# Optimization experiments

Hardware: AMD Instinct MI355X
Metric: run time of the kernel (lower is better)

Reference implementation:

```python
import jax, jax.numpy as jnp
import numpy as np

EPS = 1e-5
H = 8
N_BUCKETS = 32


def _instance_norm(x, gamma, beta):
    # x: [B, N, D]; torch InstanceNorm1d normalizes over the N (length) dim
    # per channel per batch element, using biased variance.
    m = jnp.mean(x, axis=1, keepdims=True)
    v = jnp.var(x, axis=1, keepdims=True)
    return (x - m) * jax.lax.rsqrt(v + EPS) * gamma + beta


def setup_inputs() -> dict:
    key = jax.random.key(0)
    ks = jax.random.split(key, 12)
    B, N, D, d_ff = 4, 512, 128, 512
    s = 1.0 / np.sqrt(D)
    sf = 1.0 / np.sqrt(d_ff)
    u = lambda k, shape, lim: jax.random.uniform(k, shape, jnp.float32, -lim, lim)
    return {
        "h": jax.random.normal(ks[0], (B, N, D), jnp.float32),
        "coords": jax.random.uniform(ks[1], (B, N, 2), jnp.float32),
        "W_Q": u(ks[2], (D, D), s),
        "W_K": u(ks[3], (D, D), s),
        "W_V": u(ks[4], (D, D), s),
        "W_O": u(ks[5], (D, D), s),
        "emb": jax.random.normal(ks[6], (N_BUCKETS, D), jnp.float32),  # n_heads*d_k == D
        "ffn_w1": u(ks[7], (D, d_ff), s),
        "ffn_b1": u(ks[8], (d_ff,), s),
        "ffn_w2": u(ks[9], (d_ff, D), sf),
        "ffn_b2": u(ks[10], (D,), sf),
        "gamma1": jnp.ones((D,), jnp.float32),
        "beta1": jnp.zeros((D,), jnp.float32),
        "gamma2": jnp.ones((D,), jnp.float32),
        "beta2": jnp.zeros((D,), jnp.float32),
    }


def reference(h, coords, W_Q, W_K, W_V, W_O, emb, ffn_w1, ffn_b1, ffn_w2,
              ffn_b2, gamma1, beta1, gamma2, beta2):
    B, N, D = h.shape
    Dk = D // H
    Q = (h @ W_Q).reshape(B, N, H, Dk)
    K = (h @ W_K).reshape(B, N, H, Dk)
    V = (h @ W_V).reshape(B, N, H, Dk)
    # content scores: [B, H, N, N]
    scores = jnp.einsum('bnhd,bmhd->bhnm', Q, K) / np.sqrt(Dk)
    # relative-distance bucket embeddings for all (i, j) pairs
    diff = coords[:, :, None, :] - coords[:, None, :, :]          # [B,N,N,2]
    dist = jax.lax.stop_gradient(jnp.sqrt(jnp.sum(diff * diff, -1)))
    buckets = jnp.clip((dist * N_BUCKETS).astype(jnp.int32), 0, N_BUCKETS - 1)
    r = emb[buckets].reshape(B, N, N, H, Dk)                      # [B,N,N,H,Dk]
    scores = scores + jnp.einsum('bnhd,bnmhd->bhnm', Q, r)
    attn = jax.nn.softmax(scores, axis=-1)
    h_attn = jnp.einsum('bhnm,bmhd->bnhd', attn, V).reshape(B, N, D) @ W_O
    h1 = _instance_norm(h + h_attn, gamma1, beta1)
    h_ffn = jax.nn.relu(h1 @ ffn_w1 + ffn_b1) @ ffn_w2 + ffn_b2
    return _instance_norm(h1 + h_ffn, gamma2, beta2)
```

## Files before the change

### kernel.cpp

```cpp
#include <hip/hip_runtime.h>
#include <hip/hip_bf16.h>

#define B_  4
#define N_  512
#define D_  128
#define H_  8
#define DK  16
#define DFF 512
#define NB  32
#define KS  8
#define FS  8

__global__ __launch_bounds__(256) void qkv_qe_kernel(
    const float* __restrict__ A,
    const float* __restrict__ WQ, const float* __restrict__ WK, const float* __restrict__ WV,
    const float* __restrict__ emb,
    float* __restrict__ Qo, float* __restrict__ Ko, float* __restrict__ Vo,
    float* __restrict__ QE)
{
    const float* Bw = blockIdx.z == 0 ? WQ : (blockIdx.z == 1 ? WK : WV);
    float*       C  = blockIdx.z == 0 ? Qo : (blockIdx.z == 1 ? Ko : Vo);
    const int wave = threadIdx.x >> 6;
    const int lane = threadIdx.x & 63;
    const int rbase = __builtin_amdgcn_readfirstlane((blockIdx.x * 4 + wave) * 4);
    const int col = lane * 2;

    float acc[4][2] = {};
#pragma unroll 2
    for (int k0 = 0; k0 < D_; k0 += 4) {
        float4 a4[4];
#pragma unroll
        for (int j = 0; j < 4; ++j)
            a4[j] = *(const float4*)&A[(size_t)(rbase + j) * D_ + k0];
#pragma unroll
        for (int kk = 0; kk < 4; ++kk) {
            float2 bv = *(const float2*)&Bw[(size_t)(k0 + kk) * D_ + col];
#pragma unroll
            for (int j = 0; j < 4; ++j) {
                float a = (&a4[j].x)[kk];
                acc[j][0] += a * bv.x;
                acc[j][1] += a * bv.y;
            }
        }
    }
#pragma unroll
    for (int j = 0; j < 4; ++j)
        *(float2*)&C[(size_t)(rbase + j) * D_ + col] = make_float2(acc[j][0], acc[j][1]);

    if (blockIdx.z == 0) {
        __shared__ float Qls[16][132];
#pragma unroll
        for (int j = 0; j < 4; ++j)
            *(float2*)&Qls[wave * 4 + j][col] = make_float2(acc[j][0], acc[j][1]);
        __syncthreads();
        const int r  = threadIdx.x >> 4;
        const int hh = (threadIdx.x & 15) >> 1;
        const int k0 = (threadIdx.x & 1) * 16;
        const int grow = blockIdx.x * 16 + r;
        const float4* qv = (const float4*)&Qls[r][hh * DK];
        const float4 qa = qv[0], qb = qv[1], qc = qv[2], qd = qv[3];
        float* qe_out = QE + ((size_t)grow * H_ + hh) * NB + k0;
#pragma unroll 4
        for (int k = 0; k < 16; ++k) {
            const float4* ep = (const float4*)(emb + (size_t)(k0 + k) * D_ + hh * DK);
            float4 e0 = ep[0], e1 = ep[1], e2 = ep[2], e3 = ep[3];
            float dot = qa.x*e0.x + qa.y*e0.y + qa.z*e0.z + qa.w*e0.w
                      + qb.x*e1.x + qb.y*e1.y + qb.z*e1.z + qb.w*e1.w
                      + qc.x*e2.x + qc.y*e2.y + qc.z*e2.z + qc.w*e2.w
                      + qd.x*e3.x + qd.y*e3.y + qd.z*e3.z + qd.w*e3.w;
            qe_out[k] = dot;
        }
    }
}

__global__ __launch_bounds__(256) void attn5_kernel(
    const float* __restrict__ Q, const float* __restrict__ K, const float* __restrict__ V,
    const float* __restrict__ QE, const float* __restrict__ coords,
    float* __restrict__ P)
{
    const int tid  = threadIdx.x;
    const int wave = tid >> 6;
    const int lane = tid & 63;
    const int bid  = blockIdx.x;
    const int ks    = bid & 7;
    const int chunk = (bid >> 3) & 7;
    const int h     = (bid >> 6) & (H_ - 1);
    const int b     = bid >> 9;

    const int n   = chunk * 64 + lane;
    const int row = b * N_ + n;

    __shared__ float qel[64][NB + 1];
    __shared__ float ckrd[64][2];
    __shared__ float accl[4][64][17];

    {
        int r = tid >> 2, part = tid & 3;
        const float* src = QE + ((size_t)(b * N_ + chunk * 64 + r) * H_ + h) * NB + part * 8;
#pragma unroll
        for (int j = 0; j < 8; ++j) qel[r][part * 8 + j] = src[j];
    }
    if (tid < 128)
        ((float*)ckrd)[tid] = coords[(size_t)(b * N_ + ks * 64) * 2 + tid];

    const float4* qp = (const float4*)(Q + (size_t)row * D_ + h * DK);
    const float4 q0 = qp[0], q1 = qp[1], q2 = qp[2], q3 = qp[3];
    const float cx = coords[(size_t)row * 2 + 0];
    const float cy = coords[(size_t)row * 2 + 1];

    __syncthreads();

    const size_t hdbase = (size_t)b * N_ * D_ + h * DK;

    float l = 0.f;
    float acc[16] = {};

    const int m0 = __builtin_amdgcn_readfirstlane(ks * 64 + wave * 16);
#pragma unroll 4
    for (int i = 0; i < 16; ++i) {
        const int m = m0 + i;
        const float4* kp = (const float4*)(K + hdbase + (size_t)m * D_);
        const float4 k0 = kp[0], k1 = kp[1], k2 = kp[2], k3 = kp[3];
        float dot = q0.x*k0.x + q0.y*k0.y + q0.z*k0.z + q0.w*k0.w
                  + q1.x*k1.x + q1.y*k1.y + q1.z*k1.z + q1.w*k1.w
                  + q2.x*k2.x + q2.y*k2.y + q2.z*k2.z + q2.w*k2.w
                  + q3.x*k3.x + q3.y*k3.y + q3.z*k3.z + q3.w*k3.w;
        const int mloc = m - ks * 64;
        float dx = cx - ckrd[mloc][0], dy = cy - ckrd[mloc][1];
        float dist = sqrtf(dx * dx + dy * dy);
        int bucket = (int)(dist * 32.0f);
        bucket = bucket > (NB - 1) ? (NB - 1) : bucket;
        float s = dot * 0.25f + qel[lane][bucket];
        float p = __expf(s);
        l += p;
        const float4* vp = (const float4*)(V + hdbase + (size_t)m * D_);
        const float4 v0 = vp[0], v1 = vp[1], v2 = vp[2], v3 = vp[3];
        acc[0]  += p * v0.x; acc[1]  += p * v0.y; acc[2]  += p * v0.z; acc[3]  += p * v0.w;
        acc[4]  += p * v1.x; acc[5]  += p * v1.y; acc[6]  += p * v1.z; acc[7]  += p * v1.w;
        acc[8]  += p * v2.x; acc[9]  += p * v2.y; acc[10] += p * v2.z; acc[11] += p * v2.w;
        acc[12] += p * v3.x; acc[13] += p * v3.y; acc[14] += p * v3.z; acc[15] += p * v3.w;
    }

    accl[wave][lane][16] = l;
#pragma unroll
    for (int j = 0; j < 16; ++j) accl[wave][lane][j] = acc[j];
    __syncthreads();

    float* pb = P + (size_t)bid * (64 * 17);
    for (int i = tid; i < 64 * 17; i += 256) {
        int r = i / 17, j = i - r * 17;
        pb[i] = accl[0][r][j] + accl[1][r][j] + accl[2][r][j] + accl[3][r][j];
    }
}

__global__ __launch_bounds__(256) void oproj_kernel(
    const float* __restrict__ P, const float* __restrict__ WO,
    const float* __restrict__ hres, float* __restrict__ X1)
{
    const int tid = threadIdx.x;
    const int gr0 = blockIdx.x * 16;
    __shared__ float AOls[16][128];
    __shared__ float lsl[16][8];

    if (tid < 128) {
        int r = tid >> 3, hh = tid & 7;
        int gr = gr0 + r;
        int b = gr >> 9, n = gr & (N_ - 1);
        int chunk = n >> 6, rl = n & 63;
        size_t base = ((size_t)(((b * H_ + hh) * 8 + chunk) * KS)) * (64 * 17) + (size_t)rl * 17;
        float l = 0.f;
#pragma unroll
        for (int s = 0; s < KS; ++s) l += P[base + (size_t)s * (64 * 17) + 16];
        lsl[r][hh] = l;
    }

    float asum[8];
#pragma unroll
    for (int j = 0; j < 8; ++j) {
        int i = tid + j * 256;
        int r = i >> 7, d = i & 127;
        int gr = gr0 + r;
        int b = gr >> 9, n = gr & (N_ - 1);
        int chunk = n >> 6, rl = n & 63;
        int hh = d >> 4, dk = d & 15;
        size_t base = ((size_t)(((b * H_ + hh) * 8 + chunk) * KS)) * (64 * 17) + (size_t)rl * 17 + dk;
        float a = 0.f;
#pragma unroll
        for (int s = 0; s < KS; ++s) a += P[base + (size_t)s * (64 * 17)];
        asum[j] = a;
    }
    __syncthreads();
#pragma unroll
    for (int j = 0; j < 8; ++j) {
        int i = tid + j * 256;
        int r = i >> 7, d = i & 127;
        AOls[r][d] = asum[j] / lsl[r][d >> 4];
    }
    __syncthreads();

    const int wave = tid >> 6;
    const int lane = tid & 63;
    const int rl = wave * 4;
    const int grb = __builtin_amdgcn_readfirstlane(gr0 + rl);
    const int col = lane * 2;

    float acc[4][2] = {};
#pragma unroll 2
    for (int k0 = 0; k0 < D_; k0 += 4) {
        float4 a4[4];
#pragma unroll
        for (int j = 0; j < 4; ++j) a4[j] = *(const float4*)&AOls[rl + j][k0];
#pragma unroll
        for (int kk = 0; kk < 4; ++kk) {
            float2 bv = *(const float2*)&WO[(size_t)(k0 + kk) * D_ + col];
#pragma unroll
            for (int j = 0; j < 4; ++j) {
                float a = (&a4[j].x)[kk];
                acc[j][0] += a * bv.x;
                acc[j][1] += a * bv.y;
            }
        }
    }
#pragma unroll
    for (int j = 0; j < 4; ++j) {
        float2 rv = *(const float2*)&hres[(size_t)(grb + j) * D_ + col];
        *(float2*)&X1[(size_t)(grb + j) * D_ + col] =
            make_float2(acc[j][0] + rv.x, acc[j][1] + rv.y);
    }
}

__global__ __launch_bounds__(256) void stats_kernel(const float* __restrict__ X,
    const float* __restrict__ gamma, const float* __restrict__ beta,
    float* __restrict__ T1, float* __restrict__ T2)
{
    const int b  = blockIdx.x >> 3;
    const int dg = blockIdx.x & 7;
    const int dl = threadIdx.x & 15;
    const int nc = threadIdx.x >> 4;
    const int d  = dg * 16 + dl;
    const float* xb = X + (size_t)b * N_ * D_ + d;
    float s = 0.f, q = 0.f;
    for (int i = 0; i < 32; ++i) {
        float x = xb[(size_t)(nc * 32 + i) * D_];
        s += x; q += x * x;
    }
    __shared__ float ls[16][17], lq[16][17];
    ls[nc][dl] = s; lq[nc][dl] = q;
    __syncthreads();
    if (threadIdx.x < 16) {
        float S = 0.f, Q2 = 0.f;
#pragma unroll
        for (int i = 0; i < 16; ++i) { S += ls[i][threadIdx.x]; Q2 += lq[i][threadIdx.x]; }
        int dd = dg * 16 + threadIdx.x;
        float mean = S * (1.0f / N_);
        float var  = Q2 * (1.0f / N_) - mean * mean;
        float r = 1.0f / sqrtf(var + 1e-5f);
        float t1 = r * gamma[dd];
        T1[b * D_ + dd] = t1;
        T2[b * D_ + dd] = beta[dd] - mean * t1;
    }
}

__global__ __launch_bounds__(256) void ffn1_kernel(
    const float* __restrict__ X1, const float* __restrict__ T1, const float* __restrict__ T2,
    const float* __restrict__ w1, const float* __restrict__ b1, float* __restrict__ F1)
{
    __shared__ float Als[32][128];
    const int gr0 = blockIdx.x * 32;
    const int b = gr0 >> 9;
    for (int i = threadIdx.x * 4; i < 32 * 128; i += 1024) {
        int r = i >> 7, c = i & 127;
        float4 x  = *(const float4*)&X1[(size_t)(gr0 + r) * D_ + c];
        float4 t1 = *(const float4*)&T1[b * D_ + c];
        float4 t2 = *(const float4*)&T2[b * D_ + c];
        float4 y;
        y.x = x.x * t1.x + t2.x; y.y = x.y * t1.y + t2.y;
        y.z = x.z * t1.z + t2.z; y.w = x.w * t1.w + t2.w;
        *(float4*)&Als[r][c] = y;
    }
    __syncthreads();

    const int wave = threadIdx.x >> 6;
    const int lane = threadIdx.x & 63;
    const int rl = wave * 8;
    const int grb = __builtin_amdgcn_readfirstlane(gr0 + rl);
    const int col = blockIdx.y * 128 + lane * 2;

    float acc[8][2] = {};
#pragma unroll 2
    for (int k0 = 0; k0 < D_; k0 += 4) {
        float4 a4[8];
#pragma unroll
        for (int j = 0; j < 8; ++j) a4[j] = *(const float4*)&Als[rl + j][k0];
#pragma unroll
        for (int kk = 0; kk < 4; ++kk) {
            float2 bv = *(const float2*)&w1[(size_t)(k0 + kk) * DFF + col];
#pragma unroll
            for (int j = 0; j < 8; ++j) {
                float a = (&a4[j].x)[kk];
                acc[j][0] += a * bv.x;
                acc[j][1] += a * bv.y;
            }
        }
    }
    float2 bb = *(const float2*)&b1[col];
#pragma unroll
    for (int j = 0; j < 8; ++j) {
        float o0 = fmaxf(acc[j][0] + bb.x, 0.f);
        float o1 = fmaxf(acc[j][1] + bb.y, 0.f);
        *(float2*)&F1[(size_t)(grb + j) * DFF + col] = make_float2(o0, o1);
    }
}

__global__ __launch_bounds__(256) void ffn2s_kernel(
    const float* __restrict__ F1, const float* __restrict__ w2, float* __restrict__ Pf)
{
    const int wave = threadIdx.x >> 6;
    const int lane = threadIdx.x & 63;
    const int rbase = __builtin_amdgcn_readfirstlane((blockIdx.x * 4 + wave) * 8);
    const int col = lane * 2;
    const int s = blockIdx.z;
    const int kbeg = s * (DFF / FS);

    float acc[8][2] = {};
#pragma unroll 2
    for (int k0 = kbeg; k0 < kbeg + DFF / FS; k0 += 4) {
        float4 a4[8];
#pragma unroll
        for (int j = 0; j < 8; ++j)
            a4[j] = *(const float4*)&F1[(size_t)(rbase + j) * DFF + k0];
#pragma unroll
        for (int kk = 0; kk < 4; ++kk) {
            float2 bv = *(const float2*)&w2[(size_t)(k0 + kk) * D_ + col];
#pragma unroll
            for (int j = 0; j < 8; ++j) {
                float a = (&a4[j].x)[kk];
                acc[j][0] += a * bv.x;
                acc[j][1] += a * bv.y;
            }
        }
    }
#pragma unroll
    for (int j = 0; j < 8; ++j)
        *(float2*)&Pf[((size_t)s * (B_ * N_) + rbase + j) * D_ + col] =
            make_float2(acc[j][0], acc[j][1]);
}

__global__ __launch_bounds__(256) void fcomb_kernel(
    const float* __restrict__ Pf, const float* __restrict__ b2,
    const float* __restrict__ X1, const float* __restrict__ T1, const float* __restrict__ T2,
    float* __restrict__ X2)
{
    int idx = (blockIdx.x * 256 + threadIdx.x) * 4;
    int d = idx & (D_ - 1);
    int b = idx >> 16;
    float4 o  = *(const float4*)&b2[d];
    float4 x1 = *(const float4*)&X1[idx];
    float4 t1 = *(const float4*)&T1[b * D_ + d];
    float4 t2 = *(const float4*)&T2[b * D_ + d];
    o.x += x1.x * t1.x + t2.x; o.y += x1.y * t1.y + t2.y;
    o.z += x1.z * t1.z + t2.z; o.w += x1.w * t1.w + t2.w;
#pragma unroll
    for (int s = 0; s < FS; ++s) {
        float4 p = *(const float4*)&Pf[(size_t)s * (B_ * N_ * D_) + idx];
        o.x += p.x; o.y += p.y; o.z += p.z; o.w += p.w;
    }
    *(float4*)&X2[idx] = o;
}

__global__ __launch_bounds__(256) void stats_apply_kernel(const float* __restrict__ X,
    const float* __restrict__ gamma, const float* __restrict__ beta,
    float* __restrict__ Y)
{
    const int b  = blockIdx.x >> 3;
    const int dg = blockIdx.x & 7;
    const int dl = threadIdx.x & 15;
    const int nc = threadIdx.x >> 4;
    const int d  = dg * 16 + dl;
    const float* xb = X + (size_t)b * N_ * D_ + d;
    float s = 0.f, q = 0.f;
#pragma unroll 4
    for (int i = 0; i < 32; ++i) {
        float x = xb[(size_t)(nc * 32 + i) * D_];
        s += x; q += x * x;
    }
    __shared__ float ls[16][17], lq[16][17];
    __shared__ float t1l[16], t2l[16];
    ls[nc][dl] = s; lq[nc][dl] = q;
    __syncthreads();
    if (threadIdx.x < 16) {
        float S = 0.f, Q2 = 0.f;
#pragma unroll
        for (int i = 0; i < 16; ++i) { S += ls[i][threadIdx.x]; Q2 += lq[i][threadIdx.x]; }
        int dd = dg * 16 + threadIdx.x;
        float mean = S * (1.0f / N_);
        float var  = Q2 * (1.0f / N_) - mean * mean;
        float r = 1.0f / sqrtf(var + 1e-5f);
        float t1 = r * gamma[dd];
        t1l[threadIdx.x] = t1;
        t2l[threadIdx.x] = beta[dd] - mean * t1;
    }
    __syncthreads();
    const float t1 = t1l[dl], t2 = t2l[dl];
    float* yb = Y + (size_t)b * N_ * D_ + d;
#pragma unroll 4
    for (int i = 0; i < 32; ++i) {
        size_t off = (size_t)(nc * 32 + i) * D_;
        yb[off] = xb[off] * t1 + t2;
    }
}

extern "C" void kernel_launch(void* const* d_in, const int* in_sizes, int n_in,
                              void* d_out, int out_size, void* d_ws, size_t ws_size,
                              hipStream_t stream)
{
    const float* h      = (const float*)d_in[0];
    const float* coords = (const float*)d_in[1];
    const float* W_Q    = (const float*)d_in[2];
    const float* W_K    = (const float*)d_in[3];
    const float* W_V    = (const float*)d_in[4];
    const float* W_O    = (const float*)d_in[5];
    const float* emb    = (const float*)d_in[6];
    const float* w1     = (const float*)d_in[7];
    const float* b1     = (const float*)d_in[8];
    const float* w2     = (const float*)d_in[9];
    const float* b2     = (const float*)d_in[10];
    const float* g1     = (const float*)d_in[11];
    const float* be1    = (const float*)d_in[12];
    const float* g2     = (const float*)d_in[13];
    const float* be2    = (const float*)d_in[14];
    float* out = (float*)d_out;

    float* ws = (float*)d_ws;
    const size_t R = (size_t)B_ * N_;
    float* Qb  = ws;
    float* Kb  = Qb + R * D_;
    float* Vb  = Kb + R * D_;
    float* QEb = Vb + R * D_;
    float* X1  = QEb + R * H_ * NB;
    float* F1  = X1 + R * D_;
    float* X2  = F1 + R * DFF;
    float* Pb  = X2 + R * D_;
    float* Pf  = Pb + (size_t)2048 * 64 * 17;
    float* T1a = Pf + (size_t)FS * R * D_;
    float* T2a = T1a + B_ * D_;

    qkv_qe_kernel<<<dim3(128, 1, 3), 256, 0, stream>>>(
        h, W_Q, W_K, W_V, emb, Qb, Kb, Vb, QEb);
    attn5_kernel<<<dim3(2048), 256, 0, stream>>>(Qb, Kb, Vb, QEb, coords, Pb);
    oproj_kernel<<<dim3((int)R / 16), 256, 0, stream>>>(Pb, W_O, h, X1);
    stats_kernel<<<dim3(B_ * 8), 256, 0, stream>>>(X1, g1, be1, T1a, T2a);
    ffn1_kernel<<<dim3(64, 4), 256, 0, stream>>>(X1, T1a, T2a, w1, b1, F1);
    ffn2s_kernel<<<dim3(64, 1, FS), 256, 0, stream>>>(F1, w2, Pf);
    fcomb_kernel<<<dim3((int)(R * D_) / 1024), 256, 0, stream>>>(Pf, b2, X1, T1a, T2a, X2);
    stats_apply_kernel<<<dim3(B_ * 8), 256, 0, stream>>>(X2, g2, be2, out);
}
```

Measured before the change: 86.62 us.

## Shrink per-block rows across kernels, stage K/V in LDS, widen norm stats grid

```diff
diff --git a/kernel.cpp b/kernel.cpp
--- a/kernel.cpp
+++ b/kernel.cpp
@@ -22,46 +22,39 @@
     float*       C  = blockIdx.z == 0 ? Qo : (blockIdx.z == 1 ? Ko : Vo);
     const int wave = threadIdx.x >> 6;
     const int lane = threadIdx.x & 63;
-    const int rbase = __builtin_amdgcn_readfirstlane((blockIdx.x * 4 + wave) * 4);
+    const int rbase = __builtin_amdgcn_readfirstlane((blockIdx.x * 4 + wave) * 2);
     const int col = lane * 2;
 
-    float acc[4][2] = {};
+    float acc[2][2] = {};
 #pragma unroll 2
     for (int k0 = 0; k0 < D_; k0 += 4) {
-        float4 a4[4];
-#pragma unroll
-        for (int j = 0; j < 4; ++j)
-            a4[j] = *(const float4*)&A[(size_t)(rbase + j) * D_ + k0];
+        float4 a0 = *(const float4*)&A[(size_t)(rbase + 0) * D_ + k0];
+        float4 a1 = *(const float4*)&A[(size_t)(rbase + 1) * D_ + k0];
 #pragma unroll
         for (int kk = 0; kk < 4; ++kk) {
             float2 bv = *(const float2*)&Bw[(size_t)(k0 + kk) * D_ + col];
-#pragma unroll
-            for (int j = 0; j < 4; ++j) {
-                float a = (&a4[j].x)[kk];
-                acc[j][0] += a * bv.x;
-                acc[j][1] += a * bv.y;
-            }
+            float x0 = (&a0.x)[kk], x1 = (&a1.x)[kk];
+            acc[0][0] += x0 * bv.x; acc[0][1] += x0 * bv.y;
+            acc[1][0] += x1 * bv.x; acc[1][1] += x1 * bv.y;
         }
     }
-#pragma unroll
-    for (int j = 0; j < 4; ++j)
-        *(float2*)&C[(size_t)(rbase + j) * D_ + col] = make_float2(acc[j][0], acc[j][1]);
+    *(float2*)&C[(size_t)(rbase + 0) * D_ + col] = make_float2(acc[0][0], acc[0][1]);
+    *(float2*)&C[(size_t)(rbase + 1) * D_ + col] = make_float2(acc[1][0], acc[1][1]);
 
     if (blockIdx.z == 0) {
-        __shared__ float Qls[16][132];
-#pragma unroll
-        for (int j = 0; j < 4; ++j)
-            *(float2*)&Qls[wave * 4 + j][col] = make_float2(acc[j][0], acc[j][1]);
+        __shared__ float Qls[8][132];
+        *(float2*)&Qls[wave * 2 + 0][col] = make_float2(acc[0][0], acc[0][1]);
+        *(float2*)&Qls[wave * 2 + 1][col] = make_float2(acc[1][0], acc[1][1]);
         __syncthreads();
-        const int r  = threadIdx.x >> 4;
-        const int hh = (threadIdx.x & 15) >> 1;
-        const int k0 = (threadIdx.x & 1) * 16;
-        const int grow = blockIdx.x * 16 + r;
+        const int r  = threadIdx.x >> 5;
+        const int hh = (threadIdx.x >> 2) & 7;
+        const int k0 = (threadIdx.x & 3) * 8;
+        const int grow = blockIdx.x * 8 + r;
         const float4* qv = (const float4*)&Qls[r][hh * DK];
         const float4 qa = qv[0], qb = qv[1], qc = qv[2], qd = qv[3];
         float* qe_out = QE + ((size_t)grow * H_ + hh) * NB + k0;
-#pragma unroll 4
-        for (int k = 0; k < 16; ++k) {
+#pragma unroll 2
+        for (int k = 0; k < 8; ++k) {
             const float4* ep = (const float4*)(emb + (size_t)(k0 + k) * D_ + hh * DK);
             float4 e0 = ep[0], e1 = ep[1], e2 = ep[2], e3 = ep[3];
             float dot = qa.x*e0.x + qa.y*e0.y + qa.z*e0.z + qa.w*e0.w
@@ -73,7 +66,7 @@
     }
 }
 
-__global__ __launch_bounds__(256) void attn5_kernel(
+__global__ __launch_bounds__(256) void attn6_kernel(
     const float* __restrict__ Q, const float* __restrict__ K, const float* __restrict__ V,
     const float* __restrict__ QE, const float* __restrict__ coords,
     float* __restrict__ P)
@@ -90,10 +83,20 @@
     const int n   = chunk * 64 + lane;
     const int row = b * N_ + n;
 
+    __shared__ float kl[64][16];
+    __shared__ float vl[64][16];
     __shared__ float qel[64][NB + 1];
     __shared__ float ckrd[64][2];
     __shared__ float accl[4][64][17];
 
+    const size_t hdbase = (size_t)b * N_ * D_ + h * DK;
+
+    {
+        int key = tid >> 2, part = tid & 3;
+        size_t g = hdbase + (size_t)(ks * 64 + key) * D_ + part * 4;
+        *(float4*)&kl[key][part * 4] = *(const float4*)&K[g];
+        *(float4*)&vl[key][part * 4] = *(const float4*)&V[g];
+    }
     {
         int r = tid >> 2, part = tid & 3;
         const float* src = QE + ((size_t)(b * N_ + chunk * 64 + r) * H_ + h) * NB + part * 8;
@@ -110,30 +113,27 @@
 
     __syncthreads();
 
-    const size_t hdbase = (size_t)b * N_ * D_ + h * DK;
-
     float l = 0.f;
     float acc[16] = {};
 
-    const int m0 = __builtin_amdgcn_readfirstlane(ks * 64 + wave * 16);
+    const int ml0 = wave * 16;
 #pragma unroll 4
     for (int i = 0; i < 16; ++i) {
-        const int m = m0 + i;
-        const float4* kp = (const float4*)(K + hdbase + (size_t)m * D_);
+        const int ml = ml0 + i;
+        const float4* kp = (const float4*)&kl[ml][0];
         const float4 k0 = kp[0], k1 = kp[1], k2 = kp[2], k3 = kp[3];
         float dot = q0.x*k0.x + q0.y*k0.y + q0.z*k0.z + q0.w*k0.w
                   + q1.x*k1.x + q1.y*k1.y + q1.z*k1.z + q1.w*k1.w
                   + q2.x*k2.x + q2.y*k2.y + q2.z*k2.z + q2.w*k2.w
                   + q3.x*k3.x + q3.y*k3.y + q3.z*k3.z + q3.w*k3.w;
-        const int mloc = m - ks * 64;
-        float dx = cx - ckrd[mloc][0], dy = cy - ckrd[mloc][1];
+        float dx = cx - ckrd[ml][0], dy = cy - ckrd[ml][1];
         float dist = sqrtf(dx * dx + dy * dy);
         int bucket = (int)(dist * 32.0f);
         bucket = bucket > (NB - 1) ? (NB - 1) : bucket;
         float s = dot * 0.25f + qel[lane][bucket];
         float p = __expf(s);
         l += p;
-        const float4* vp = (const float4*)(V + hdbase + (size_t)m * D_);
+        const float4* vp = (const float4*)&vl[ml][0];
         const float4 v0 = vp[0], v1 = vp[1], v2 = vp[2], v3 = vp[3];
         acc[0]  += p * v0.x; acc[1]  += p * v0.y; acc[2]  += p * v0.z; acc[3]  += p * v0.w;
         acc[4]  += p * v1.x; acc[5]  += p * v1.y; acc[6]  += p * v1.z; acc[7]  += p * v1.w;
@@ -158,11 +158,11 @@
     const float* __restrict__ hres, float* __restrict__ X1)
 {
     const int tid = threadIdx.x;
-    const int gr0 = blockIdx.x * 16;
-    __shared__ float AOls[16][128];
-    __shared__ float lsl[16][8];
-
-    if (tid < 128) {
+    const int gr0 = blockIdx.x * 8;
+    __shared__ float AOls[8][128];
+    __shared__ float lsl[8][8];
+
+    if (tid < 64) {
         int r = tid >> 3, hh = tid & 7;
         int gr = gr0 + r;
         int b = gr >> 9, n = gr & (N_ - 1);
@@ -174,9 +174,9 @@
         lsl[r][hh] = l;
     }
 
-    float asum[8];
-#pragma unroll
-    for (int j = 0; j < 8; ++j) {
+    float asum[4];
+#pragma unroll
+    for (int j = 0; j < 4; ++j) {
         int i = tid + j * 256;
         int r = i >> 7, d = i & 127;
         int gr = gr0 + r;
@@ -191,7 +191,7 @@
     }
     __syncthreads();
 #pragma unroll
-    for (int j = 0; j < 8; ++j) {
+    for (int j = 0; j < 4; ++j) {
         int i = tid + j * 256;
         int r = i >> 7, d = i & 127;
         AOls[r][d] = asum[j] / lsl[r][d >> 4];
@@ -200,29 +200,25 @@
 
     const int wave = tid >> 6;
     const int lane = tid & 63;
-    const int rl = wave * 4;
+    const int rl = wave * 2;
     const int grb = __builtin_amdgcn_readfirstlane(gr0 + rl);
     const int col = lane * 2;
 
-    float acc[4][2] = {};
+    float acc[2][2] = {};
 #pragma unroll 2
     for (int k0 = 0; k0 < D_; k0 += 4) {
-        float4 a4[4];
-#pragma unroll
-        for (int j = 0; j < 4; ++j) a4[j] = *(const float4*)&AOls[rl + j][k0];
+        float4 a0 = *(const float4*)&AOls[rl + 0][k0];
+        float4 a1 = *(const float4*)&AOls[rl + 1][k0];
 #pragma unroll
         for (int kk = 0; kk < 4; ++kk) {
             float2 bv = *(const float2*)&WO[(size_t)(k0 + kk) * D_ + col];
-#pragma unroll
-            for (int j = 0; j < 4; ++j) {
-                float a = (&a4[j].x)[kk];
-                acc[j][0] += a * bv.x;
-                acc[j][1] += a * bv.y;
-            }
+            float x0 = (&a0.x)[kk], x1 = (&a1.x)[kk];
+            acc[0][0] += x0 * bv.x; acc[0][1] += x0 * bv.y;
+            acc[1][0] += x1 * bv.x; acc[1][1] += x1 * bv.y;
         }
     }
 #pragma unroll
-    for (int j = 0; j < 4; ++j) {
+    for (int j = 0; j < 2; ++j) {
         float2 rv = *(const float2*)&hres[(size_t)(grb + j) * D_ + col];
         *(float2*)&X1[(size_t)(grb + j) * D_ + col] =
             make_float2(acc[j][0] + rv.x, acc[j][1] + rv.y);
@@ -233,31 +229,29 @@
     const float* __restrict__ gamma, const float* __restrict__ beta,
     float* __restrict__ T1, float* __restrict__ T2)
 {
-    const int b  = blockIdx.x >> 3;
-    const int dg = blockIdx.x & 7;
-    const int dl = threadIdx.x & 15;
-    const int nc = threadIdx.x >> 4;
-    const int d  = dg * 16 + dl;
-    const float* xb = X + (size_t)b * N_ * D_ + d;
+    const int b  = blockIdx.x >> 5;
+    const int dg = blockIdx.x & 31;
+    const int dl = threadIdx.x & 3;
+    const int nc = threadIdx.x >> 2;
+    const float* xp = X + ((size_t)b * N_ + nc * 8) * D_ + dg * 4 + dl;
     float s = 0.f, q = 0.f;
-    for (int i = 0; i < 32; ++i) {
-        float x = xb[(size_t)(nc * 32 + i) * D_];
-        s += x; q += x * x;
-    }
-    __shared__ float ls[16][17], lq[16][17];
-    ls[nc][dl] = s; lq[nc][dl] = q;
-    __syncthreads();
-    if (threadIdx.x < 16) {
-        float S = 0.f, Q2 = 0.f;
-#pragma unroll
-        for (int i = 0; i < 16; ++i) { S += ls[i][threadIdx.x]; Q2 += lq[i][threadIdx.x]; }
-        int dd = dg * 16 + threadIdx.x;
-        float mean = S * (1.0f / N_);
-        float var  = Q2 * (1.0f / N_) - mean * mean;
+#pragma unroll
+    for (int i = 0; i < 8; ++i) { float x = xp[(size_t)i * D_]; s += x; q += x * x; }
+    __shared__ float rs[64][4], rq[64][4];
+    rs[nc][dl] = s; rq[nc][dl] = q;
+    __syncthreads();
+    for (int off = 32; off >= 1; off >>= 1) {
+        if (nc < off) { rs[nc][dl] += rs[nc + off][dl]; rq[nc][dl] += rq[nc + off][dl]; }
+        __syncthreads();
+    }
+    if (threadIdx.x < 4) {
+        int d = dg * 4 + threadIdx.x;
+        float mean = rs[0][threadIdx.x] * (1.0f / N_);
+        float var  = rq[0][threadIdx.x] * (1.0f / N_) - mean * mean;
         float r = 1.0f / sqrtf(var + 1e-5f);
-        float t1 = r * gamma[dd];
-        T1[b * D_ + dd] = t1;
-        T2[b * D_ + dd] = beta[dd] - mean * t1;
+        float t1 = r * gamma[d];
+        T1[b * D_ + d] = t1;
+        T2[b * D_ + d] = beta[d] - mean * t1;
     }
 }
 
@@ -265,10 +259,11 @@
     const float* __restrict__ X1, const float* __restrict__ T1, const float* __restrict__ T2,
     const float* __restrict__ w1, const float* __restrict__ b1, float* __restrict__ F1)
 {
-    __shared__ float Als[32][128];
-    const int gr0 = blockIdx.x * 32;
+    __shared__ float Als[16][128];
+    const int gr0 = blockIdx.x * 16;
     const int b = gr0 >> 9;
-    for (int i = threadIdx.x * 4; i < 32 * 128; i += 1024) {
+#pragma unroll
+    for (int i = threadIdx.x * 4; i < 16 * 128; i += 1024) {
         int r = i >> 7, c = i & 127;
         float4 x  = *(const float4*)&X1[(size_t)(gr0 + r) * D_ + c];
         float4 t1 = *(const float4*)&T1[b * D_ + c];
@@ -282,21 +277,21 @@
 
     const int wave = threadIdx.x >> 6;
     const int lane = threadIdx.x & 63;
-    const int rl = wave * 8;
+    const int rl = wave * 4;
     const int grb = __builtin_amdgcn_readfirstlane(gr0 + rl);
     const int col = blockIdx.y * 128 + lane * 2;
 
-    float acc[8][2] = {};
+    float acc[4][2] = {};
 #pragma unroll 2
     for (int k0 = 0; k0 < D_; k0 += 4) {
-        float4 a4[8];
-#pragma unroll
-        for (int j = 0; j < 8; ++j) a4[j] = *(const float4*)&Als[rl + j][k0];
+        float4 a4[4];
+#pragma unroll
+        for (int j = 0; j < 4; ++j) a4[j] = *(const float4*)&Als[rl + j][k0];
 #pragma unroll
         for (int kk = 0; kk < 4; ++kk) {
             float2 bv = *(const float2*)&w1[(size_t)(k0 + kk) * DFF + col];
 #pragma unroll
-            for (int j = 0; j < 8; ++j) {
+            for (int j = 0; j < 4; ++j) {
                 float a = (&a4[j].x)[kk];
                 acc[j][0] += a * bv.x;
                 acc[j][1] += a * bv.y;
@@ -305,7 +300,7 @@
     }
     float2 bb = *(const float2*)&b1[col];
 #pragma unroll
-    for (int j = 0; j < 8; ++j) {
+    for (int j = 0; j < 4; ++j) {
         float o0 = fmaxf(acc[j][0] + bb.x, 0.f);
         float o1 = fmaxf(acc[j][1] + bb.y, 0.f);
         *(float2*)&F1[(size_t)(grb + j) * DFF + col] = make_float2(o0, o1);
@@ -317,23 +312,23 @@
 {
     const int wave = threadIdx.x >> 6;
     const int lane = threadIdx.x & 63;
-    const int rbase = __builtin_amdgcn_readfirstlane((blockIdx.x * 4 + wave) * 8);
+    const int rbase = __builtin_amdgcn_readfirstlane((blockIdx.x * 4 + wave) * 4);
     const int col = lane * 2;
     const int s = blockIdx.z;
     const int kbeg = s * (DFF / FS);
 
-    float acc[8][2] = {};
+    float acc[4][2] = {};
 #pragma unroll 2
     for (int k0 = kbeg; k0 < kbeg + DFF / FS; k0 += 4) {
-        float4 a4[8];
-#pragma unroll
-        for (int j = 0; j < 8; ++j)
+        float4 a4[4];
+#pragma unroll
+        for (int j = 0; j < 4; ++j)
             a4[j] = *(const float4*)&F1[(size_t)(rbase + j) * DFF + k0];
 #pragma unroll
         for (int kk = 0; kk < 4; ++kk) {
             float2 bv = *(const float2*)&w2[(size_t)(k0 + kk) * D_ + col];
 #pragma unroll
-            for (int j = 0; j < 8; ++j) {
+            for (int j = 0; j < 4; ++j) {
                 float a = (&a4[j].x)[kk];
                 acc[j][0] += a * bv.x;
                 acc[j][1] += a * bv.y;
@@ -341,7 +336,7 @@
         }
     }
 #pragma unroll
-    for (int j = 0; j < 8; ++j)
+    for (int j = 0; j < 4; ++j)
         *(float2*)&Pf[((size_t)s * (B_ * N_) + rbase + j) * D_ + col] =
             make_float2(acc[j][0], acc[j][1]);
 }
@@ -372,42 +367,36 @@
     const float* __restrict__ gamma, const float* __restrict__ beta,
     float* __restrict__ Y)
 {
-    const int b  = blockIdx.x >> 3;
-    const int dg = blockIdx.x & 7;
-    const int dl = threadIdx.x & 15;
-    const int nc = threadIdx.x >> 4;
-    const int d  = dg * 16 + dl;
-    const float* xb = X + (size_t)b * N_ * D_ + d;
+    const int b  = blockIdx.x >> 5;
+    const int dg = blockIdx.x & 31;
+    const int dl = threadIdx.x & 3;
+    const int nc = threadIdx.x >> 2;
+    const float* xp = X + ((size_t)b * N_ + nc * 8) * D_ + dg * 4 + dl;
     float s = 0.f, q = 0.f;
-#pragma unroll 4
-    for (int i = 0; i < 32; ++i) {
-        float x = xb[(size_t)(nc * 32 + i) * D_];
-        s += x; q += x * x;
-    }
-    __shared__ float ls[16][17], lq[16][17];
-    __shared__ float t1l[16], t2l[16];
-    ls[nc][dl] = s; lq[nc][dl] = q;
-    __syncthreads();
-    if (threadIdx.x < 16) {
-        float S = 0.f, Q2 = 0.f;
-#pragma unroll
-        for (int i = 0; i < 16; ++i) { S += ls[i][threadIdx.x]; Q2 += lq[i][threadIdx.x]; }
-        int dd = dg * 16 + threadIdx.x;
-        float mean = S * (1.0f / N_);
-        float var  = Q2 * (1.0f / N_) - mean * mean;
+#pragma unroll
+    for (int i = 0; i < 8; ++i) { float x = xp[(size_t)i * D_]; s += x; q += x * x; }
+    __shared__ float rs[64][4], rq[64][4];
+    __shared__ float t1l[4], t2l[4];
+    rs[nc][dl] = s; rq[nc][dl] = q;
+    __syncthreads();
+    for (int off = 32; off >= 1; off >>= 1) {
+        if (nc < off) { rs[nc][dl] += rs[nc + off][dl]; rq[nc][dl] += rq[nc + off][dl]; }
+        __syncthreads();
+    }
+    if (threadIdx.x < 4) {
+        int d = dg * 4 + threadIdx.x;
+        float mean = rs[0][threadIdx.x] * (1.0f / N_);
+        float var  = rq[0][threadIdx.x] * (1.0f / N_) - mean * mean;
         float r = 1.0f / sqrtf(var + 1e-5f);
-        float t1 = r * gamma[dd];
+        float t1 = r * gamma[d];
         t1l[threadIdx.x] = t1;
-        t2l[threadIdx.x] = beta[dd] - mean * t1;
+        t2l[threadIdx.x] = beta[d] - mean * t1;
     }
     __syncthreads();
     const float t1 = t1l[dl], t2 = t2l[dl];
-    float* yb = Y + (size_t)b * N_ * D_ + d;
-#pragma unroll 4
-    for (int i = 0; i < 32; ++i) {
-        size_t off = (size_t)(nc * 32 + i) * D_;
-        yb[off] = xb[off] * t1 + t2;
-    }
+    float* yp = Y + ((size_t)b * N_ + nc * 8) * D_ + dg * 4 + dl;
+#pragma unroll
+    for (int i = 0; i < 8; ++i) yp[(size_t)i * D_] = xp[(size_t)i * D_] * t1 + t2;
 }
 
 extern "C" void kernel_launch(void* const* d_in, const int* in_sizes, int n_in,
@@ -445,13 +434,13 @@
     float* T1a = Pf + (size_t)FS * R * D_;
     float* T2a = T1a + B_ * D_;
 
-    qkv_qe_kernel<<<dim3(128, 1, 3), 256, 0, stream>>>(
+    qkv_qe_kernel<<<dim3(256, 1, 3), 256, 0, stream>>>(
         h, W_Q, W_K, W_V, emb, Qb, Kb, Vb, QEb);
-    attn5_kernel<<<dim3(2048), 256, 0, stream>>>(Qb, Kb, Vb, QEb, coords, Pb);
-    oproj_kernel<<<dim3((int)R / 16), 256, 0, stream>>>(Pb, W_O, h, X1);
-    stats_kernel<<<dim3(B_ * 8), 256, 0, stream>>>(X1, g1, be1, T1a, T2a);
-    ffn1_kernel<<<dim3(64, 4), 256, 0, stream>>>(X1, T1a, T2a, w1, b1, F1);
-    ffn2s_kernel<<<dim3(64, 1, FS), 256, 0, stream>>>(F1, w2, Pf);
+    attn6_kernel<<<dim3(2048), 256, 0, stream>>>(Qb, Kb, Vb, QEb, coords, Pb);
+    oproj_kernel<<<dim3((int)R / 8), 256, 0, stream>>>(Pb, W_O, h, X1);
+    stats_kernel<<<dim3(B_ * 32), 256, 0, stream>>>(X1, g1, be1, T1a, T2a);
+    ffn1_kernel<<<dim3(128, 4), 256, 0, stream>>>(X1, T1a, T2a, w1, b1, F1);
+    ffn2s_kernel<<<dim3(128, 1, FS), 256, 0, stream>>>(F1, w2, Pf);
     fcomb_kernel<<<dim3((int)(R * D_) / 1024), 256, 0, stream>>>(Pf, b2, X1, T1a, T2a, X2);
-    stats_apply_kernel<<<dim3(B_ * 8), 256, 0, stream>>>(X2, g2, be2, out);
-}
+    stats_apply_kernel<<<dim3(B_ * 32), 256, 0, stream>>>(X2, g2, be2, out);
+}
```

Result: faster. 84.56 us (-2.4%).
